# Kernel optimization log

Hardware: AMD Instinct MI355X
Metric: run time of the kernel (lower is better)

The kernel has to match this reference:

```python
import jax, jax.numpy as jnp
import numpy as np
import math

D_MODEL = 512
D_STATE = 16
D_CONV = 4
EXPAND = 2
D_INNER = EXPAND * D_MODEL          # 1024
D_HALF = D_INNER // 2               # 512
DT_RANK = math.ceil(D_MODEL / 16)   # 32
BATCH, SEQLEN = 2, 4096
DT_MIN, DT_MAX, DT_FLOOR = 0.001, 0.1, 1e-4


def setup_inputs() -> dict:
    key = jax.random.key(0)
    ks = jax.random.split(key, 9)

    def lin(k, fan_out, fan_in):
        return jax.random.normal(k, (fan_out, fan_in), jnp.float32) / np.float32(np.sqrt(fan_in))

    hidden_states = jax.random.normal(ks[0], (BATCH, SEQLEN, D_MODEL), jnp.float32)
    in_proj_w = lin(ks[1], D_INNER, D_MODEL)
    x_proj_w = lin(ks[2], DT_RANK + 2 * D_STATE, D_HALF)
    dt_std = np.float32(DT_RANK ** -0.5)
    dt_proj_w = jax.random.uniform(ks[3], (D_HALF, DT_RANK), jnp.float32, -dt_std, dt_std)
    dt = jnp.exp(jax.random.uniform(ks[4], (D_HALF,), jnp.float32)
                 * (math.log(DT_MAX) - math.log(DT_MIN)) + math.log(DT_MIN))
    dt = jnp.clip(dt, DT_FLOOR)
    dt_proj_b = dt + jnp.log(-jnp.expm1(-dt))  # inverse-softplus init
    A_log = jnp.log(jnp.tile(jnp.arange(1, D_STATE + 1, dtype=jnp.float32)[None, :], (D_HALF, 1)))
    D = jnp.ones((D_HALF,), jnp.float32)
    out_proj_w = lin(ks[5], D_MODEL, D_INNER)
    conv1d_x_w = jax.random.normal(ks[6], (D_HALF, 1, D_CONV), jnp.float32) / np.float32(np.sqrt(D_CONV))
    conv1d_z_w = jax.random.normal(ks[7], (D_HALF, 1, D_CONV), jnp.float32) / np.float32(np.sqrt(D_CONV))
    return dict(hidden_states=hidden_states, in_proj_w=in_proj_w,
                conv1d_x_w=conv1d_x_w, conv1d_z_w=conv1d_z_w,
                x_proj_w=x_proj_w, dt_proj_w=dt_proj_w, dt_proj_b=dt_proj_b,
                A_log=A_log, D=D, out_proj_w=out_proj_w)


def _dwconv_same(x, w):
    # x: (b, c, l); w: (c, 1, k) depthwise. torch padding='same' with k=4 pads (1, 2),
    # which matches lax 'SAME'.
    return jax.lax.conv_general_dilated(
        x, w, window_strides=(1,), padding='SAME',
        dimension_numbers=('NCH', 'OIH', 'NCH'),
        feature_group_count=x.shape[1])


def _selective_scan(x, delta, A, B, C, D):
    # x, delta: (b, d, l); A: (d, n); B, C: (b, n, l); D: (d,)
    dA = jnp.exp(jnp.einsum('bdl,dn->bldn', delta, A))        # (b, l, d, n)
    dBx = jnp.einsum('bdl,bnl,bdl->bldn', delta, B, x)        # (b, l, d, n)

    def combine(c1, c2):
        a1, b1 = c1
        a2, b2 = c2
        return a1 * a2, a2 * b1 + b2

    _, h = jax.lax.associative_scan(combine, (dA, dBx), axis=1)  # h: (b, l, d, n)
    y = jnp.einsum('bldn,bnl->bdl', h, C) + D[None, :, None] * x
    return y


def reference(hidden_states, in_proj_w, conv1d_x_w, conv1d_z_w, x_proj_w,
              dt_proj_w, dt_proj_b, A_log, D, out_proj_w):
    b, l, _ = hidden_states.shape
    xz = jnp.einsum('bld,ed->bel', hidden_states, in_proj_w)   # (b, d_inner, l)
    x, z = jnp.split(xz, 2, axis=1)                            # each (b, d_half, l)
    A = -jnp.exp(A_log.astype(jnp.float32))
    x = jax.nn.silu(_dwconv_same(x, conv1d_x_w))
    z = jax.nn.silu(_dwconv_same(z, conv1d_z_w))
    x_dbl = jnp.einsum('bdl,ed->bel', x, x_proj_w)             # (b, dt_rank+2n, l)
    dt_r = x_dbl[:, :DT_RANK]                                  # (b, dt_rank, l)
    Bm = x_dbl[:, DT_RANK:DT_RANK + D_STATE]                   # (b, n, l)
    Cm = x_dbl[:, DT_RANK + D_STATE:]                          # (b, n, l)
    dt = jnp.einsum('brl,dr->bdl', dt_r, dt_proj_w)            # (b, d_half, l)
    delta = jax.nn.softplus(dt + dt_proj_b.astype(jnp.float32)[None, :, None])
    y = _selective_scan(x, delta, A, Bm, Cm, D.astype(jnp.float32))
    y = jnp.concatenate([y, z], axis=1)                        # (b, d_inner, l)
    out = jnp.einsum('bdl,ed->ble', y, out_proj_w)             # (b, l, d_model)
    return out
```

## Files before the change

### kernel.cpp

```cpp
#include <hip/hip_runtime.h>
#include <math.h>

#define BB 2
#define LL 4096
#define DMODEL 512
#define DINNER 1024
#define DHALF 512
#define DSTATE 16
#define RK 32
#define NCH 64
#define NC 256
#define CLEN (LL/NC)
#define NG 16
#define GL (NC/NG)
#define LOG2E 1.44269504088896f

typedef __attribute__((ext_vector_type(8))) short short8;
typedef __attribute__((ext_vector_type(4))) float f32x4;

__device__ __forceinline__ float silu_f(float v) { return v / (1.f + __expf(-v)); }

__device__ __forceinline__ unsigned short f2bf(float x) {
    unsigned int u = __float_as_uint(x);
    u += 0x7fffu + ((u >> 16) & 1u);
    return (unsigned short)(u >> 16);
}
__device__ __forceinline__ float bf2f(unsigned short u) {
    return __uint_as_float((unsigned int)u << 16);
}

__device__ __forceinline__ float softplus_f(float x) {
    return fmaxf(x, 0.f) + __logf(1.f + __expf(-fabsf(x)));
}

__device__ __forceinline__ float exp2_raw(float x) { return __builtin_amdgcn_exp2f(x); }

__device__ __forceinline__ void gload16(const unsigned short* g, unsigned short* l) {
    __builtin_amdgcn_global_load_lds((const __attribute__((address_space(1))) void*)g,
                                     (__attribute__((address_space(3))) void*)l, 16, 0, 0);
}

#define H4  1048576
#define W14 131072
#define W24 131072
#define W34 8192
__global__ void cast_all(const float* __restrict__ hid, const float* __restrict__ w1,
                         const float* __restrict__ w2, const float* __restrict__ w3,
                         unsigned short* __restrict__ Hb, unsigned short* __restrict__ Wb,
                         unsigned short* __restrict__ Wob, unsigned short* __restrict__ Wxb) {
    int i = blockIdx.x * 256 + threadIdx.x;
    const float* src; unsigned short* dst; int j;
    if (i < H4)                    { src = hid; dst = Hb;  j = i; }
    else if (i < H4 + W14)         { src = w1;  dst = Wb;  j = i - H4; }
    else if (i < H4 + W14 + W24)   { src = w2;  dst = Wob; j = i - H4 - W14; }
    else if (i < H4 + W14 + W24 + W34) { src = w3; dst = Wxb; j = i - H4 - W14 - W24; }
    else return;
    float4 v = *(const float4*)&src[(size_t)j * 4];
    ushort4 o = make_ushort4(f2bf(v.x), f2bf(v.y), f2bf(v.z), f2bf(v.w));
    *(ushort4*)&dst[(size_t)j * 4] = o;
}

template<int K, int E, bool BF16OUT>
__global__ __launch_bounds__(256) void gemm_mfma(const unsigned short* __restrict__ W,
                                                 const unsigned short* __restrict__ X,
                                                 void* __restrict__ outv) {
    __shared__ unsigned short Wa[128 * 64];
    __shared__ unsigned short Xa[128 * 64];
    const int tid = threadIdx.x;
    const int lane = tid & 63;
    const int w = tid >> 6;
    const int wr = w >> 1, wc = w & 1;
    const int frow = lane & 15;
    const int kg = lane >> 4;
    const int e0 = blockIdx.y * 128;
    const int r0 = blockIdx.x * 128;

    f32x4 acc[4][4] = {};

    for (int kt = 0; kt < K / 64; ++kt) {
        #pragma unroll
        for (int i = 0; i < 4; ++i) {
            int flat = i * 256 + tid;
            int row = flat >> 3;
            int slot = flat & 7;
            int chunk = slot ^ (row & 7);
            gload16(&W[(size_t)(e0 + row) * K + kt * 64 + chunk * 8], &Wa[flat * 8]);
            gload16(&X[(size_t)(r0 + row) * K + kt * 64 + chunk * 8], &Xa[flat * 8]);
        }
        __syncthreads();

        #pragma unroll
        for (int ks = 0; ks < 2; ++ks) {
            short8 af[4], bfr[4];
            #pragma unroll
            for (int m = 0; m < 4; ++m) {
                int row = wr * 64 + m * 16 + frow;
                int phys = (ks * 4 + kg) ^ (row & 7);
                af[m] = *(const short8*)&Wa[row * 64 + phys * 8];
            }
            #pragma unroll
            for (int n = 0; n < 4; ++n) {
                int row = wc * 64 + n * 16 + frow;
                int phys = (ks * 4 + kg) ^ (row & 7);
                bfr[n] = *(const short8*)&Xa[row * 64 + phys * 8];
            }
            #pragma unroll
            for (int m = 0; m < 4; ++m)
                #pragma unroll
                for (int n = 0; n < 4; ++n)
                    acc[m][n] = __builtin_amdgcn_mfma_f32_16x16x32_bf16(af[m], bfr[n], acc[m][n], 0, 0, 0);
        }
        __syncthreads();
    }

    #pragma unroll
    for (int m = 0; m < 4; ++m) {
        #pragma unroll
        for (int n = 0; n < 4; ++n) {
            int e = e0 + wr * 64 + m * 16 + kg * 4;
            int r = r0 + wc * 64 + n * 16 + frow;
            f32x4 a = acc[m][n];
            if constexpr (BF16OUT) {
                ushort4 o = make_ushort4(f2bf(a.x), f2bf(a.y), f2bf(a.z), f2bf(a.w));
                *(ushort4*)&((unsigned short*)outv)[(size_t)r * E + e] = o;
            } else {
                *(f32x4*)&((float*)outv)[(size_t)r * E + e] = a;
            }
        }
    }
}

__global__ __launch_bounds__(256) void gemm_xproj(const unsigned short* __restrict__ W,
                                                  const unsigned short* __restrict__ X,
                                                  float* __restrict__ out) {
    __shared__ unsigned short Xa[128 * 64];
    __shared__ unsigned short Wa[64 * 64];
    const int tid = threadIdx.x;
    const int lane = tid & 63;
    const int w = tid >> 6;
    const int frow = lane & 15;
    const int kg = lane >> 4;
    const int r0 = blockIdx.x * 128;

    f32x4 acc[4][2] = {};

    for (int kt = 0; kt < 512 / 64; ++kt) {
        #pragma unroll
        for (int i = 0; i < 4; ++i) {
            int flat = i * 256 + tid;
            int row = flat >> 3;
            int slot = flat & 7;
            int chunk = slot ^ (row & 7);
            gload16(&X[(size_t)(r0 + row) * 512 + kt * 64 + chunk * 8], &Xa[flat * 8]);
        }
        #pragma unroll
        for (int i = 0; i < 2; ++i) {
            int flat = i * 256 + tid;
            int row = flat >> 3;
            int slot = flat & 7;
            int chunk = slot ^ (row & 7);
            gload16(&W[(size_t)row * 512 + kt * 64 + chunk * 8], &Wa[flat * 8]);
        }
        __syncthreads();

        #pragma unroll
        for (int ks = 0; ks < 2; ++ks) {
            short8 af[4], bfr[2];
            #pragma unroll
            for (int m = 0; m < 4; ++m) {
                int row = m * 16 + frow;
                int phys = (ks * 4 + kg) ^ (row & 7);
                af[m] = *(const short8*)&Wa[row * 64 + phys * 8];
            }
            #pragma unroll
            for (int n = 0; n < 2; ++n) {
                int row = w * 32 + n * 16 + frow;
                int phys = (ks * 4 + kg) ^ (row & 7);
                bfr[n] = *(const short8*)&Xa[row * 64 + phys * 8];
            }
            #pragma unroll
            for (int m = 0; m < 4; ++m)
                #pragma unroll
                for (int n = 0; n < 2; ++n)
                    acc[m][n] = __builtin_amdgcn_mfma_f32_16x16x32_bf16(af[m], bfr[n], acc[m][n], 0, 0, 0);
        }
        __syncthreads();
    }

    #pragma unroll
    for (int m = 0; m < 4; ++m) {
        #pragma unroll
        for (int n = 0; n < 2; ++n) {
            int r = r0 + w * 32 + n * 16 + frow;
            int b = r >> 12;
            int l = r & (LL - 1);
            int e = m * 16 + kg * 4;
            #pragma unroll
            for (int i = 0; i < 4; ++i)
                out[((size_t)b * NCH + e + i) * LL + l] = acc[m][n][i];
        }
    }
}

__global__ void conv_silu(const unsigned short* __restrict__ xzb,
                          const float* __restrict__ wx, const float* __restrict__ wz,
                          unsigned short* __restrict__ xqb, unsigned short* __restrict__ ycb) {
    __shared__ float s[67][64];
    const int b = blockIdx.z;
    const int l0 = blockIdx.x * 64;
    const int c0 = blockIdx.y * 64;
    const int tid = threadIdx.x;
    for (int idx = tid; idx < 67 * 16; idx += 256) {
        int rr = idx >> 4, u = idx & 15;
        int l = l0 - 1 + rr;
        float4 f;
        if (l >= 0 && l < LL) {
            ushort4 v = *(const ushort4*)&xzb[((size_t)b * LL + l) * DINNER + c0 + u * 4];
            f = make_float4(bf2f(v.x), bf2f(v.y), bf2f(v.z), bf2f(v.w));
        } else f = make_float4(0.f, 0.f, 0.f, 0.f);
        *(float4*)&s[rr][u * 4] = f;
    }
    __syncthreads();
    const int ct = (tid & 15) * 4;
    const int c = c0 + ct;
    const bool isx = (c < DHALF);
    const float* wp = isx ? &wx[c * 4] : &wz[(c - DHALF) * 4];
    float4 w0 = *(const float4*)&wp[0];
    float4 w1 = *(const float4*)&wp[4];
    float4 w2 = *(const float4*)&wp[8];
    float4 w3 = *(const float4*)&wp[12];
    #pragma unroll
    for (int rep = 0; rep < 4; ++rep) {
        int ll = (tid >> 4) + rep * 16;
        float4 t0 = *(const float4*)&s[ll][ct];
        float4 t1 = *(const float4*)&s[ll + 1][ct];
        float4 t2 = *(const float4*)&s[ll + 2][ct];
        float4 t3 = *(const float4*)&s[ll + 3][ct];
        float v0 = w0.x*t0.x + w0.y*t1.x + w0.z*t2.x + w0.w*t3.x;
        float v1 = w1.x*t0.y + w1.y*t1.y + w1.z*t2.y + w1.w*t3.y;
        float v2 = w2.x*t0.z + w2.y*t1.z + w2.z*t2.z + w2.w*t3.z;
        float v3 = w3.x*t0.w + w3.y*t1.w + w3.z*t2.w + w3.w*t3.w;
        ushort4 o = make_ushort4(f2bf(silu_f(v0)), f2bf(silu_f(v1)),
                                 f2bf(silu_f(v2)), f2bf(silu_f(v3)));
        int l = l0 + ll;
        if (isx) *(ushort4*)&xqb[((size_t)b * LL + l) * DHALF + c] = o;
        else     *(ushort4*)&ycb[((size_t)b * LL + l) * DINNER + c] = o;
    }
}

__global__ __launch_bounds__(256, 4) void scan1(const unsigned short* __restrict__ xqb,
                      const float* __restrict__ xdbl, const float* __restrict__ A_log,
                      const float* __restrict__ dtw, const float* __restrict__ dtb,
                      float* __restrict__ pend, float* __restrict__ hend) {
    __shared__ float s[48][CLEN];
    const int b = blockIdx.z;
    const int d = blockIdx.y * 256 + threadIdx.x;
    const int c = blockIdx.x;
    const int tid = threadIdx.x;
    for (int idx = tid; idx < 48 * CLEN; idx += 256) {
        int ch = idx >> 4, ll = idx & (CLEN - 1);
        s[ch][ll] = xdbl[((size_t)b * NCH + ch) * LL + c * CLEN + ll];
    }
    float dtwreg[RK];
    #pragma unroll
    for (int r = 0; r < RK; r += 4) {
        float4 v = *(const float4*)&dtw[d * RK + r];
        dtwreg[r] = v.x; dtwreg[r+1] = v.y; dtwreg[r+2] = v.z; dtwreg[r+3] = v.w;
    }
    float Arow2[DSTATE];
    #pragma unroll
    for (int n = 0; n < DSTATE; ++n) Arow2[n] = -expf(A_log[d * DSTATE + n]) * LOG2E;
    const float bias = dtb[d];
    float del[CLEN];
    #pragma unroll
    for (int t = 0; t < CLEN; ++t) del[t] = bias;
    __syncthreads();
    #pragma unroll
    for (int r = 0; r < RK; ++r) {
        float wv = dtwreg[r];
        #pragma unroll
        for (int q = 0; q < CLEN / 4; ++q) {
            float4 v = *(const float4*)&s[r][q * 4];
            del[q*4+0] = fmaf(v.x, wv, del[q*4+0]);
            del[q*4+1] = fmaf(v.y, wv, del[q*4+1]);
            del[q*4+2] = fmaf(v.z, wv, del[q*4+2]);
            del[q*4+3] = fmaf(v.w, wv, del[q*4+3]);
        }
    }
    float sdel = 0.f;
    #pragma unroll
    for (int t = 0; t < CLEN; ++t) { del[t] = softplus_f(del[t]); sdel += del[t]; }

    float h[DSTATE];
    #pragma unroll
    for (int n = 0; n < DSTATE; ++n) h[n] = 0.f;
    #pragma unroll
    for (int t = 0; t < CLEN; ++t) {
        float dl = del[t];
        float xv = bf2f(xqb[((size_t)b * LL + c * CLEN + t) * DHALF + d]);
        float dx = dl * xv;
        #pragma unroll
        for (int n = 0; n < DSTATE; ++n) {
            float dA = exp2_raw(dl * Arow2[n]);
            h[n] = fmaf(dA, h[n], dx * s[32 + n][t]);
        }
    }
    size_t base = (((size_t)b * NC + c) * DSTATE) * DHALF + d;
    #pragma unroll
    for (int n = 0; n < DSTATE; ++n) {
        pend[base + (size_t)n * DHALF] = exp2_raw(Arow2[n] * sdel);
        hend[base + (size_t)n * DHALF] = h[n];
    }
}

__global__ void scan2a(float* __restrict__ pend, float* __restrict__ hend,
                       float* __restrict__ gP, float* __restrict__ gH) {
    int flat = blockIdx.x * 256 + threadIdx.x;
    int d = flat & (DHALF - 1);
    int n = (flat >> 9) & (DSTATE - 1);
    int g = (flat >> 13) & (NG - 1);
    int b = flat >> 17;
    const size_t stride = (size_t)DSTATE * DHALF;
    size_t idx = (((size_t)b * NC + g * GL) * DSTATE + n) * DHALF + d;
    float P = 1.f, H = 0.f;
    #pragma unroll
    for (int j = 0; j < GL; ++j) {
        float p = pend[idx], h = hend[idx];
        pend[idx] = P; hend[idx] = H;
        H = fmaf(p, H, h);
        P *= p;
        idx += stride;
    }
    size_t gi = (((size_t)b * NG + g) * DSTATE + n) * DHALF + d;
    gP[gi] = P; gH[gi] = H;
}

__global__ void scan2b(const float* __restrict__ gP, float* __restrict__ gH) {
    int flat = blockIdx.x * 256 + threadIdx.x;
    int d = flat & (DHALF - 1);
    int n = (flat >> 9) & (DSTATE - 1);
    int b = flat >> 13;
    float h = 0.f;
    const size_t stride = (size_t)DSTATE * DHALF;
    size_t gi = (((size_t)b * NG) * DSTATE + n) * DHALF + d;
    for (int g = 0; g < NG; ++g) {
        float P = gP[gi], Hh = gH[gi];
        gH[gi] = h;
        h = fmaf(P, h, Hh);
        gi += stride;
    }
}

__global__ __launch_bounds__(256, 4) void scan3(const unsigned short* __restrict__ xqb,
                      const float* __restrict__ xdbl, const float* __restrict__ A_log,
                      const float* __restrict__ dtw, const float* __restrict__ dtb,
                      const float* __restrict__ Dp, const float* __restrict__ pend,
                      const float* __restrict__ hend, const float* __restrict__ gH,
                      unsigned short* __restrict__ ycb) {
    __shared__ float s[64][CLEN];
    const int b = blockIdx.z;
    const int d = blockIdx.y * 256 + threadIdx.x;
    const int c = blockIdx.x;
    const int tid = threadIdx.x;
    for (int idx = tid; idx < 64 * CLEN; idx += 256) {
        int ch = idx >> 4, ll = idx & (CLEN - 1);
        s[ch][ll] = xdbl[((size_t)b * NCH + ch) * LL + c * CLEN + ll];
    }
    float dtwreg[RK];
    #pragma unroll
    for (int r = 0; r < RK; r += 4) {
        float4 v = *(const float4*)&dtw[d * RK + r];
        dtwreg[r] = v.x; dtwreg[r+1] = v.y; dtwreg[r+2] = v.z; dtwreg[r+3] = v.w;
    }
    float Arow2[DSTATE], h[DSTATE];
    size_t base = (((size_t)b * NC + c) * DSTATE) * DHALF + d;
    size_t gbase = (((size_t)b * NG + (c / GL)) * DSTATE) * DHALF + d;
    #pragma unroll
    for (int n = 0; n < DSTATE; ++n) {
        Arow2[n] = -expf(A_log[d * DSTATE + n]) * LOG2E;
        h[n] = fmaf(pend[base + (size_t)n * DHALF], gH[gbase + (size_t)n * DHALF],
                    hend[base + (size_t)n * DHALF]);
    }
    const float bias = dtb[d];
    const float Dv = Dp[d];
    float del[CLEN];
    #pragma unroll
    for (int t = 0; t < CLEN; ++t) del[t] = bias;
    __syncthreads();
    #pragma unroll
    for (int r = 0; r < RK; ++r) {
        float wv = dtwreg[r];
        #pragma unroll
        for (int q = 0; q < CLEN / 4; ++q) {
            float4 v = *(const float4*)&s[r][q * 4];
            del[q*4+0] = fmaf(v.x, wv, del[q*4+0]);
            del[q*4+1] = fmaf(v.y, wv, del[q*4+1]);
            del[q*4+2] = fmaf(v.z, wv, del[q*4+2]);
            del[q*4+3] = fmaf(v.w, wv, del[q*4+3]);
        }
    }
    #pragma unroll
    for (int t = 0; t < CLEN; ++t) del[t] = softplus_f(del[t]);

    #pragma unroll
    for (int t = 0; t < CLEN; ++t) {
        float dl = del[t];
        float xv = bf2f(xqb[((size_t)b * LL + c * CLEN + t) * DHALF + d]);
        float dx = dl * xv;
        float y = Dv * xv;
        #pragma unroll
        for (int n = 0; n < DSTATE; ++n) {
            float dA = exp2_raw(dl * Arow2[n]);
            h[n] = fmaf(dA, h[n], dx * s[32 + n][t]);
            y = fmaf(h[n], s[48 + n][t], y);
        }
        ycb[((size_t)b * LL + c * CLEN + t) * DINNER + d] = f2bf(y);
    }
}

extern "C" void kernel_launch(void* const* d_in, const int* in_sizes, int n_in,
                              void* d_out, int out_size, void* d_ws, size_t ws_size,
                              hipStream_t stream) {
    const float* hidden     = (const float*)d_in[0];
    const float* in_proj_w  = (const float*)d_in[1];
    const float* conv_x_w   = (const float*)d_in[2];
    const float* conv_z_w   = (const float*)d_in[3];
    const float* x_proj_w   = (const float*)d_in[4];
    const float* dt_proj_w  = (const float*)d_in[5];
    const float* dt_proj_b  = (const float*)d_in[6];
    const float* A_log      = (const float*)d_in[7];
    const float* Dp         = (const float*)d_in[8];
    const float* out_proj_w = (const float*)d_in[9];
    float* out = (float*)d_out;

    float* ws_f = (float*)d_ws;
    unsigned short* Wb  = (unsigned short*)(ws_f + 0);
    unsigned short* Wob = (unsigned short*)(ws_f + 262144);
    unsigned short* Wxb = (unsigned short*)(ws_f + 524288);
    unsigned short* Hb  = (unsigned short*)(ws_f + 540672);
    unsigned short* xzb = (unsigned short*)(ws_f + 2637824);
    unsigned short* xqb = (unsigned short*)(ws_f + 6832128);
    unsigned short* ycb = (unsigned short*)(ws_f + 8929280);
    float* xdbl = ws_f + 13123584;
    float* gP   = ws_f + 13647872;
    float* gH   = ws_f + 13910016;
    float* hend = ws_f + 14172160;
    float* pend = ws_f + 2637824;

    dim3 blk(256);

    cast_all<<<dim3((H4 + W14 + W24 + W34 + 255) / 256), blk, 0, stream>>>(
        hidden, in_proj_w, out_proj_w, x_proj_w, Hb, Wb, Wob, Wxb);
    gemm_mfma<DMODEL, DINNER, true><<<dim3(BB * LL / 128, DINNER / 128), blk, 0, stream>>>(Wb, Hb, xzb);
    conv_silu<<<dim3(LL / 64, DINNER / 64, BB), blk, 0, stream>>>(xzb, conv_x_w, conv_z_w, xqb, ycb);
    gemm_xproj<<<dim3(BB * LL / 128), blk, 0, stream>>>(Wxb, xqb, xdbl);
    scan1<<<dim3(NC, DHALF / 256, BB), blk, 0, stream>>>(xqb, xdbl, A_log, dt_proj_w, dt_proj_b, pend, hend);
    scan2a<<<dim3(BB * NG * DSTATE * DHALF / 256), blk, 0, stream>>>(pend, hend, gP, gH);
    scan2b<<<dim3(BB * DSTATE * DHALF / 256), blk, 0, stream>>>(gP, gH);
    scan3<<<dim3(NC, DHALF / 256, BB), blk, 0, stream>>>(xqb, xdbl, A_log, dt_proj_w, dt_proj_b,
                                                         Dp, pend, hend, gH, ycb);
    gemm_mfma<DINNER, DMODEL, false><<<dim3(BB * LL / 128, DMODEL / 128), blk, 0, stream>>>(Wob, ycb, out);
}
```

Measured before the change: 135.5 us.

## Store per-chunk delta sums instead of per-state decay products in chunked scan

```diff
diff --git a/kernel.cpp b/kernel.cpp
--- a/kernel.cpp
+++ b/kernel.cpp
@@ -251,7 +251,7 @@
 __global__ __launch_bounds__(256, 4) void scan1(const unsigned short* __restrict__ xqb,
                       const float* __restrict__ xdbl, const float* __restrict__ A_log,
                       const float* __restrict__ dtw, const float* __restrict__ dtb,
-                      float* __restrict__ pend, float* __restrict__ hend) {
+                      float* __restrict__ sdelb, float* __restrict__ hend) {
     __shared__ float s[48][CLEN];
     const int b = blockIdx.z;
     const int d = blockIdx.y * 256 + threadIdx.x;
@@ -305,34 +305,38 @@
             h[n] = fmaf(dA, h[n], dx * s[32 + n][t]);
         }
     }
+    sdelb[((size_t)b * NC + c) * DHALF + d] = sdel;
     size_t base = (((size_t)b * NC + c) * DSTATE) * DHALF + d;
     #pragma unroll
-    for (int n = 0; n < DSTATE; ++n) {
-        pend[base + (size_t)n * DHALF] = exp2_raw(Arow2[n] * sdel);
+    for (int n = 0; n < DSTATE; ++n)
         hend[base + (size_t)n * DHALF] = h[n];
-    }
-}
-
-__global__ void scan2a(float* __restrict__ pend, float* __restrict__ hend,
+}
+
+__global__ void scan2a(const float* __restrict__ sdelb, float* __restrict__ hend,
+                       const float* __restrict__ A_log,
                        float* __restrict__ gP, float* __restrict__ gH) {
     int flat = blockIdx.x * 256 + threadIdx.x;
     int d = flat & (DHALF - 1);
     int n = (flat >> 9) & (DSTATE - 1);
     int g = (flat >> 13) & (NG - 1);
     int b = flat >> 17;
+    const float Arow2 = -expf(A_log[d * DSTATE + n]) * LOG2E;
     const size_t stride = (size_t)DSTATE * DHALF;
     size_t idx = (((size_t)b * NC + g * GL) * DSTATE + n) * DHALF + d;
-    float P = 1.f, H = 0.f;
+    size_t sidx = ((size_t)b * NC + g * GL) * DHALF + d;
+    float S = 0.f, H = 0.f;
     #pragma unroll
     for (int j = 0; j < GL; ++j) {
-        float p = pend[idx], h = hend[idx];
-        pend[idx] = P; hend[idx] = H;
-        H = fmaf(p, H, h);
-        P *= p;
+        float sd = sdelb[sidx + (size_t)j * DHALF];
+        float h = hend[idx];
+        hend[idx] = H;
+        H = fmaf(exp2_raw(Arow2 * sd), H, h);
+        S += sd;
         idx += stride;
     }
     size_t gi = (((size_t)b * NG + g) * DSTATE + n) * DHALF + d;
-    gP[gi] = P; gH[gi] = H;
+    gP[gi] = exp2_raw(Arow2 * S);
+    gH[gi] = H;
 }
 
 __global__ void scan2b(const float* __restrict__ gP, float* __restrict__ gH) {
@@ -354,7 +358,7 @@
 __global__ __launch_bounds__(256, 4) void scan3(const unsigned short* __restrict__ xqb,
                       const float* __restrict__ xdbl, const float* __restrict__ A_log,
                       const float* __restrict__ dtw, const float* __restrict__ dtb,
-                      const float* __restrict__ Dp, const float* __restrict__ pend,
+                      const float* __restrict__ Dp, const float* __restrict__ sdelb,
                       const float* __restrict__ hend, const float* __restrict__ gH,
                       unsigned short* __restrict__ ycb) {
     __shared__ float s[64][CLEN];
@@ -366,6 +370,12 @@
         int ch = idx >> 4, ll = idx & (CLEN - 1);
         s[ch][ll] = xdbl[((size_t)b * NCH + ch) * LL + c * CLEN + ll];
     }
+    float Sc = 0.f;
+    {
+        const int g0 = (c / GL) * GL;
+        for (int j = g0; j < c; ++j)
+            Sc += sdelb[((size_t)b * NC + j) * DHALF + d];
+    }
     float dtwreg[RK];
     #pragma unroll
     for (int r = 0; r < RK; r += 4) {
@@ -378,7 +388,7 @@
     #pragma unroll
     for (int n = 0; n < DSTATE; ++n) {
         Arow2[n] = -expf(A_log[d * DSTATE + n]) * LOG2E;
-        h[n] = fmaf(pend[base + (size_t)n * DHALF], gH[gbase + (size_t)n * DHALF],
+        h[n] = fmaf(exp2_raw(Arow2[n] * Sc), gH[gbase + (size_t)n * DHALF],
                     hend[base + (size_t)n * DHALF]);
     }
     const float bias = dtb[d];
@@ -444,8 +454,8 @@
     float* xdbl = ws_f + 13123584;
     float* gP   = ws_f + 13647872;
     float* gH   = ws_f + 13910016;
-    float* hend = ws_f + 14172160;
-    float* pend = ws_f + 2637824;
+    float* sdel = ws_f + 540672;
+    float* hend = ws_f + 2637824;
 
     dim3 blk(256);
 
@@ -454,10 +464,10 @@
     gemm_mfma<DMODEL, DINNER, true><<<dim3(BB * LL / 128, DINNER / 128), blk, 0, stream>>>(Wb, Hb, xzb);
     conv_silu<<<dim3(LL / 64, DINNER / 64, BB), blk, 0, stream>>>(xzb, conv_x_w, conv_z_w, xqb, ycb);
     gemm_xproj<<<dim3(BB * LL / 128), blk, 0, stream>>>(Wxb, xqb, xdbl);
-    scan1<<<dim3(NC, DHALF / 256, BB), blk, 0, stream>>>(xqb, xdbl, A_log, dt_proj_w, dt_proj_b, pend, hend);
-    scan2a<<<dim3(BB * NG * DSTATE * DHALF / 256), blk, 0, stream>>>(pend, hend, gP, gH);
+    scan1<<<dim3(NC, DHALF / 256, BB), blk, 0, stream>>>(xqb, xdbl, A_log, dt_proj_w, dt_proj_b, sdel, hend);
+    scan2a<<<dim3(BB * NG * DSTATE * DHALF / 256), blk, 0, stream>>>(sdel, hend, A_log, gP, gH);
     scan2b<<<dim3(BB * DSTATE * DHALF / 256), blk, 0, stream>>>(gP, gH);
     scan3<<<dim3(NC, DHALF / 256, BB), blk, 0, stream>>>(xqb, xdbl, A_log, dt_proj_w, dt_proj_b,
-                                                         Dp, pend, hend, gH, ycb);
+                                                         Dp, sdel, hend, gH, ycb);
     gemm_mfma<DINNER, DMODEL, false><<<dim3(BB * LL / 128, DMODEL / 128), blk, 0, stream>>>(Wob, ycb, out);
 }
```

Measured after the change: 133.6 us. About the same (-1.4%).
